# Performance work log

Measured on AMD Instinct MI355X. Metric: run time of the kernel, lower is better.

Reference implementation:

```python
import jax, jax.numpy as jnp
import numpy as np

D, A, B, R, N, E, NENT, L = 128, 64, 8, 200, 100000, 800000, 50000, 2
SLOPE = (0.125 + 1.0 / 3.0) / 2.0  # RReLU eval-mode slope (lower+upper)/2
EPS = 1e-5


def _ln(x, g, b):
    mu = jnp.mean(x, axis=-1, keepdims=True)
    v = jnp.mean((x - mu) ** 2, axis=-1, keepdims=True)
    return (x - mu) * jax.lax.rsqrt(v + EPS) * g + b


def _rrelu(x):
    return jnp.where(x >= 0, x, SLOPE * x)


def setup_inputs() -> dict:
    key = jax.random.key(0)
    ks = jax.random.split(key, 32)
    s = 0.05
    inp = {
        'hidden': jax.random.normal(ks[0], (N, D), jnp.float32),
        'rel_emb': jax.random.normal(ks[1], (B * (R + 1), D), jnp.float32),
        'batch_idx': jax.random.randint(ks[2], (E,), 0, B, jnp.int32),
        'rel': jax.random.randint(ks[3], (E,), 0, R + 1, jnp.int32),
        'sub': jax.random.randint(ks[4], (E,), 0, N, jnp.int32),
        'obj': jax.random.randint(ks[5], (E,), 0, N, jnp.int32),
        'q_rel': jax.random.randint(ks[6], (B,), 0, R + 1, jnp.int32),
        'nodes_batch': jax.random.randint(ks[7], (N,), 0, B, jnp.int32),
        'nodes_ent': jax.random.randint(ks[8], (N,), 0, NENT, jnp.int32),
        # per-layer params (stacked over L); stored as [in, out]
        'Ws': jax.random.normal(ks[9], (L, D, A)) * s,
        'Wr': jax.random.normal(ks[10], (L, D, A)) * s,
        'Wqr_w': jax.random.normal(ks[11], (L, D, A)) * s,
        'Wqr_b': jnp.zeros((L, A)),
        'Walpha_w': jax.random.normal(ks[12], (L, A)) * s,
        'Walpha_b': jnp.zeros((L,)),
        'Wh': jax.random.normal(ks[13], (L, D, D)) * s,
        'rt_w': jax.random.normal(ks[14], (L, D, D)) * s,
        'rt_b': jnp.zeros((L, D)),
        'ln_g': jnp.ones((L, D)), 'ln_b': jnp.zeros((L, D)),
        'lnr_g': jnp.ones((L, D)), 'lnr_b': jnp.zeros((L, D)),
        # shared GRU (PyTorch layout: [3D, D], gates r,z,n)
        'gru_wih': jax.random.normal(ks[15], (3 * D, D)) * s,
        'gru_whh': jax.random.normal(ks[16], (3 * D, D)) * s,
        'gru_bih': jnp.zeros((3 * D,)),
        'gru_bhh': jnp.zeros((3 * D,)),
        'Wfinal': jax.random.normal(ks[17], (D,)) * s,
    }
    return inp


def _gru_step(x, h, wih, whh, bih, bhh):
    gi = x @ wih.T + bih
    gh = h @ whh.T + bhh
    i_r, i_z, i_n = jnp.split(gi, 3, axis=-1)
    h_r, h_z, h_n = jnp.split(gh, 3, axis=-1)
    r = jax.nn.sigmoid(i_r + h_r)
    z = jax.nn.sigmoid(i_z + h_z)
    n = jnp.tanh(i_n + r * h_n)
    return (1.0 - z) * n + z * h


def reference(hidden, rel_emb, Ws, Wr, Wqr_w, Wqr_b, Walpha_w, Walpha_b, Wh,
              rt_w, rt_b, ln_g, ln_b, lnr_g, lnr_b,
              gru_wih, gru_whh, gru_bih, gru_bhh, Wfinal,
              batch_idx, rel, sub, obj, q_rel, nodes_batch, nodes_ent):
    h0 = jnp.zeros_like(hidden)
    rel_flat_idx = rel + batch_idx * (R + 1)  # [E]
    q_flat_idx = q_rel + jnp.arange(B, dtype=q_rel.dtype) * (R + 1)  # [B]
    for i in range(L):
        # relation transfer + residual + LN
        re_ = jax.nn.relu(rel_emb @ rt_w[i] + rt_b[i])
        rel_emb = _ln(rel_emb + re_, lnr_g[i], lnr_b[i])
        # GNN layer: edge-wise gather
        hs = hidden[sub]                       # [E, D]
        hr = rel_emb[rel_flat_idx]             # [E, D]
        h_qr = rel_emb[q_flat_idx][batch_idx]  # [E, D]
        pre = hs @ Ws[i] + hr @ Wr[i] + h_qr @ Wqr_w[i] + Wqr_b[i]  # [E, A]
        alpha = jax.nn.sigmoid(_rrelu(pre) @ Walpha_w[i] + Walpha_b[i])  # [E]
        msg = alpha[:, None] * (hs + hr)       # [E, D]
        agg = jax.ops.segment_sum(msg, obj, num_segments=N)  # [N, D]
        hidden = _rrelu(agg @ Wh[i])
        hidden = _ln(hidden, ln_g[i], ln_b[i])
        hidden = _gru_step(hidden, h0, gru_wih, gru_whh, gru_bih, gru_bhh)
        h0 = hidden
        rel_emb = _ln(rel_emb, lnr_g[i], lnr_b[i])
    scores = hidden @ Wfinal  # [N]
    scores_all = jnp.zeros((B, NENT), dtype=scores.dtype).at[nodes_batch, nodes_ent].set(scores)
    return scores_all
```

## Files before the change

kernel.cpp:

```cpp
#include <hip/hip_runtime.h>
#include <hip/hip_bf16.h>

constexpr int DD = 128;
constexpr int AA = 64;
constexpr int GG = 384;
constexpr int XPAD = 136;
constexpr int GTS = 192;

#define SLOPE_F 0.22916666666666666f
#define LNEPS   1e-5f

typedef __attribute__((ext_vector_type(8))) short short8;
typedef __attribute__((ext_vector_type(4))) float f32x4;

static __device__ __forceinline__ float wave_sum(float v){
#pragma unroll
  for (int off = 32; off > 0; off >>= 1) v += __shfl_xor(v, off, 64);
  return v;
}
static __device__ __forceinline__ float red16(float v){
#pragma unroll
  for (int off = 1; off < 16; off <<= 1) v += __shfl_xor(v, off, 64);
  return v;
}
static __device__ __forceinline__ float sigm(float x){ return 1.0f / (1.0f + __expf(-x)); }
static __device__ __forceinline__ float fast_tanh(float x){
  float ax = fabsf(x);
  float t = __expf(-2.0f * ax);
  float r = (1.0f - t) / (1.0f + t);
  return copysignf(r, x);
}
static __device__ __forceinline__ float rrelu_f(float x){ return x >= 0.0f ? x : SLOPE_F * x; }
static __device__ __forceinline__ short bf16b(float f){
  __hip_bfloat16 h = __float2bfloat16(f);
  return *reinterpret_cast<short*>(&h);
}
static __device__ __forceinline__ float b2f_lo(unsigned int x){
  return __uint_as_float(x << 16);
}
static __device__ __forceinline__ float b2f_hi(unsigned int x){
  return __uint_as_float(x & 0xffff0000u);
}
static __device__ __forceinline__ short8 ld_frag_f32(const float* p){
  float4 f0 = *(const float4*)p;
  float4 f1 = *(const float4*)(p + 4);
  short8 v;
  v[0]=bf16b(f0.x); v[1]=bf16b(f0.y); v[2]=bf16b(f0.z); v[3]=bf16b(f0.w);
  v[4]=bf16b(f1.x); v[5]=bf16b(f1.y); v[6]=bf16b(f1.z); v[7]=bf16b(f1.w);
  return v;
}

template<bool PRE_LN>
__global__ void __launch_bounds__(256) k_rel_transfer(float* __restrict__ rel,
    const float* __restrict__ rtw, const float* __restrict__ rtb,
    const float* __restrict__ g, const float* __restrict__ b,
    const float* __restrict__ gp, const float* __restrict__ bp, int rows){
  __shared__ float xrow[4][DD];
  float* xl = xrow[threadIdx.x >> 6];
  const int lane = threadIdx.x & 63;
  int wave = (int)((blockIdx.x * blockDim.x + threadIdx.x) >> 6);
  if (wave >= rows) return;
  int row = __builtin_amdgcn_readfirstlane(wave);
  float* x = rel + (size_t)row * DD;
  float t0 = x[lane], t1 = x[64 + lane];
  if (PRE_LN){
    float mu = wave_sum(t0 + t1) * (1.0f/128.0f);
    float e0 = t0 - mu, e1 = t1 - mu;
    float var = wave_sum(e0*e0 + e1*e1) * (1.0f/128.0f);
    float rs = rsqrtf(var + LNEPS);
    t0 = e0 * rs * gp[lane]      + bp[lane];
    t1 = e1 * rs * gp[64 + lane] + bp[64 + lane];
  }
  xl[lane] = t0; xl[64 + lane] = t1;
  float y0 = 0.f, y1 = 0.f;
#pragma unroll 4
  for (int d = 0; d < DD; ++d){
    float xd = xl[d];
    y0 = fmaf(xd, rtw[d*DD + lane],      y0);
    y1 = fmaf(xd, rtw[d*DD + 64 + lane], y1);
  }
  float u0 = t0 + fmaxf(y0 + rtb[lane],      0.f);
  float u1 = t1 + fmaxf(y1 + rtb[64 + lane], 0.f);
  float mu = wave_sum(u0 + u1) * (1.0f/128.0f);
  float e0 = u0 - mu, e1 = u1 - mu;
  float var = wave_sum(e0*e0 + e1*e1) * (1.0f/128.0f);
  float rs = rsqrtf(var + LNEPS);
  x[lane]      = e0 * rs * g[lane]      + b[lane];
  x[64 + lane] = e1 * rs * g[64 + lane] + b[64 + lane];
}

__global__ void __launch_bounds__(256) k_prep_bfrag_km(const float* __restrict__ W,
    short* __restrict__ out, int C, int ldc){
  int idx = blockIdx.x * blockDim.x + threadIdx.x;
  int total = (C >> 4) * 4 * 64;
  if (idx >= total) return;
  int lane = idx & 63, ks = (idx >> 6) & 3, ct = idx >> 8;
  int k = ks*32 + ((lane >> 4) << 3);
  int c = (ct << 4) + (lane & 15);
  short8 v;
#pragma unroll
  for (int j = 0; j < 8; ++j) v[j] = bf16b(W[(size_t)(k + j)*ldc + c]);
  *reinterpret_cast<short8*>(out + (size_t)idx * 8) = v;
}

__global__ void __launch_bounds__(256) k_prep_bfrag(const float* __restrict__ W,
    short* __restrict__ out, int Nc){
  int idx = blockIdx.x * blockDim.x + threadIdx.x;
  int total = (Nc >> 4) * 4 * 64;
  if (idx >= total) return;
  int lane = idx & 63, ks = (idx >> 6) & 3, ct = idx >> 8;
  int k = ks*32 + ((lane >> 4) << 3);
  int c = (ct << 4) + (lane & 15);
  const float* src = W + (size_t)c * DD + k;
  short8 v;
#pragma unroll
  for (int j = 0; j < 8; ++j) v[j] = bf16b(src[j]);
  *reinterpret_cast<short8*>(out + (size_t)idx * 8) = v;
}

__global__ void __launch_bounds__(256) k_proj_gt(const float* __restrict__ X,
    const short* __restrict__ Bf, unsigned short* __restrict__ GT, int rows){
  const int lane = threadIdx.x & 63;
  int wave = (int)((blockIdx.x * blockDim.x + threadIdx.x) >> 6);
  int r0 = wave * 16;
  if (r0 >= rows) return;
  if (r0 + 16 > rows) r0 = rows - 16;
  r0 = __builtin_amdgcn_readfirstlane(r0);
  const int arow = lane & 15;
  const int koff = (lane >> 4) << 3;
  short8 ax[4];
#pragma unroll
  for (int ks = 0; ks < 4; ++ks){
    ax[ks] = ld_frag_f32(X + (size_t)(r0 + arow) * DD + ks*32 + koff);
    *reinterpret_cast<short8*>((short*)GT + (size_t)(r0 + arow) * GTS + 64 + ks*32 + koff) = ax[ks];
  }
  f32x4 acc[4];
#pragma unroll
  for (int ct = 0; ct < 4; ++ct){
    acc[ct] = (f32x4)0.f;
#pragma unroll
    for (int ks = 0; ks < 4; ++ks){
      short8 bw = *reinterpret_cast<const short8*>(Bf + ((size_t)(ct*4 + ks)*64 + lane)*8);
      acc[ct] = __builtin_amdgcn_mfma_f32_16x16x32_bf16(ax[ks], bw, acc[ct], 0, 0, 0);
    }
  }
#pragma unroll
  for (int ct = 0; ct < 4; ++ct){
    int col = ct*16 + (lane & 15);
#pragma unroll
    for (int reg = 0; reg < 4; ++reg){
      int row = r0 + ((lane >> 4) << 2) + reg;
      ((short*)GT)[(size_t)row*GTS + col] = bf16b(acc[ct][reg]);
    }
  }
}

__global__ void __launch_bounds__(256) k_projq(const float* __restrict__ rel,
    const float* __restrict__ Wqr, const float* __restrict__ bias,
    const int* __restrict__ q_rel, float* __restrict__ out, int Bc, int Rp1){
  const int lane = threadIdx.x & 63;
  int wave = (int)((blockIdx.x * blockDim.x + threadIdx.x) >> 6);
  if (wave >= Bc) return;
  int b = __builtin_amdgcn_readfirstlane(wave);
  int f = __builtin_amdgcn_readfirstlane(q_rel[b] + b * Rp1);
  const float* x = rel + (size_t)f * DD;
  float a = 0.f;
#pragma unroll 4
  for (int d = 0; d < DD; ++d) a = fmaf(x[d], Wqr[d*AA + lane], a);
  out[(size_t)b*AA + lane] = a + bias[lane];
}

__global__ void __launch_bounds__(256) k_hist(const int* __restrict__ obj, int* __restrict__ deg, int E){
  int idx = blockIdx.x * blockDim.x + threadIdx.x;
  if (idx < E) atomicAdd(&deg[obj[idx]], 1);
}

__global__ void __launch_bounds__(1024) k_scan1(const int* __restrict__ deg,
    int* __restrict__ row_start, int* __restrict__ bsum, int n){
  __shared__ int sm[1024];
  int t = threadIdx.x;
  int i = blockIdx.x * 1024 + t;
  int v = (i < n) ? deg[i] : 0;
  sm[t] = v; __syncthreads();
#pragma unroll
  for (int off = 1; off < 1024; off <<= 1){
    int x = (t >= off) ? sm[t - off] : 0;
    __syncthreads();
    sm[t] += x;
    __syncthreads();
  }
  if (i < n) row_start[i] = sm[t] - v;
  if (t == 1023) bsum[blockIdx.x] = sm[1023];
}

__global__ void __launch_bounds__(1024) k_scan2(int* __restrict__ bsum, int nb){
  __shared__ int sm[1024];
  int t = threadIdx.x;
  int v = (t < nb) ? bsum[t] : 0;
  sm[t] = v; __syncthreads();
#pragma unroll
  for (int off = 1; off < 1024; off <<= 1){
    int x = (t >= off) ? sm[t - off] : 0;
    __syncthreads();
    sm[t] += x;
    __syncthreads();
  }
  if (t < nb) bsum[t] = sm[t] - v;
}

__global__ void __launch_bounds__(256) k_scan3(int* __restrict__ row_start,
    const int* __restrict__ bsum, int n, int E){
  int i = blockIdx.x * blockDim.x + threadIdx.x;
  if (i < n) row_start[i] += bsum[i >> 10];
  if (i == 0) row_start[n] = E;
}

__global__ void __launch_bounds__(256) k_scatter_edges(const int* __restrict__ obj,
    const int* __restrict__ sub, const int* __restrict__ bidx,
    const int* __restrict__ reli, const int* __restrict__ row_start,
    int* __restrict__ cursor, unsigned int* __restrict__ ER, int E, int Rp1){
  int e = blockIdx.x * blockDim.x + threadIdx.x;
  if (e < E){
    int o = obj[e];
    int pos = row_start[o] + atomicAdd(&cursor[o], 1);
    int bb = bidx[e];
    unsigned rec = (unsigned)sub[e] | ((unsigned)(reli[e] + bb * Rp1) << 17)
                 | ((unsigned)bb << 28);
    ER[pos] = rec;
  }
}

__global__ void __launch_bounds__(256) k_edge_csr4(
    const unsigned short* __restrict__ GT, const unsigned short* __restrict__ RT,
    const float* __restrict__ qr,
    const float* __restrict__ wal, const float* __restrict__ walb_p,
    const unsigned int* __restrict__ ER, const int* __restrict__ row_start,
    float* __restrict__ agg, int Nn){
  const int lane = threadIdx.x & 63;
  const int g = lane >> 4;
  const int t = lane & 15;
  int wave = (int)((blockIdx.x * blockDim.x + threadIdx.x) >> 6);
  if (wave >= Nn) return;
  int o = __builtin_amdgcn_readfirstlane(wave);
  const int s0 = __builtin_amdgcn_readfirstlane(row_start[o]);
  const int s1 = __builtin_amdgcn_readfirstlane(row_start[o + 1]);
  const float4 wa4 = *reinterpret_cast<const float4*>(wal + t*4);
  const float wb = walb_p[0];
  float acc[8];
#pragma unroll
  for (int i = 0; i < 8; ++i) acc[i] = 0.f;
  for (int base = s0; base < s1; base += 8){
    int pA = base + g;
    int pB = base + g + 4;
    bool vA = pA < s1, vB = pB < s1;
    unsigned eA = ER[vA ? pA : s0];
    unsigned eB = ER[vB ? pB : s0];
    int sA = eA & 0x1FFFF, fA = (eA >> 17) & 0x7FF, bA = eA >> 28;
    int sB = eB & 0x1FFFF, fB = (eB >> 17) & 0x7FF, bB = eB >> 28;
    const unsigned short* gsA = GT + (size_t)sA * GTS;
    const unsigned short* rfA = RT + (size_t)fA * GTS;
    const unsigned short* gsB = GT + (size_t)sB * GTS;
    const unsigned short* rfB = RT + (size_t)fB * GTS;
    uint2 pgA = *reinterpret_cast<const uint2*>(gsA + t*4);
    uint2 prA = *reinterpret_cast<const uint2*>(rfA + t*4);
    float4 q4A = *reinterpret_cast<const float4*>(qr + (size_t)bA*AA + t*4);
    uint4 xgA = *reinterpret_cast<const uint4*>(gsA + 64 + t*8);
    uint4 xrA = *reinterpret_cast<const uint4*>(rfA + 64 + t*8);
    uint2 pgB = *reinterpret_cast<const uint2*>(gsB + t*4);
    uint2 prB = *reinterpret_cast<const uint2*>(rfB + t*4);
    float4 q4B = *reinterpret_cast<const float4*>(qr + (size_t)bB*AA + t*4);
    uint4 xgB = *reinterpret_cast<const uint4*>(gsB + 64 + t*8);
    uint4 xrB = *reinterpret_cast<const uint4*>(rfB + 64 + t*8);
    float pA0 = b2f_lo(pgA.x) + b2f_lo(prA.x) + q4A.x;
    float pA1 = b2f_hi(pgA.x) + b2f_hi(prA.x) + q4A.y;
    float pA2 = b2f_lo(pgA.y) + b2f_lo(prA.y) + q4A.z;
    float pA3 = b2f_hi(pgA.y) + b2f_hi(prA.y) + q4A.w;
    float dotA = rrelu_f(pA0)*wa4.x + rrelu_f(pA1)*wa4.y
               + rrelu_f(pA2)*wa4.z + rrelu_f(pA3)*wa4.w;
    float pB0 = b2f_lo(pgB.x) + b2f_lo(prB.x) + q4B.x;
    float pB1 = b2f_hi(pgB.x) + b2f_hi(prB.x) + q4B.y;
    float pB2 = b2f_lo(pgB.y) + b2f_lo(prB.y) + q4B.z;
    float pB3 = b2f_hi(pgB.y) + b2f_hi(prB.y) + q4B.w;
    float dotB = rrelu_f(pB0)*wa4.x + rrelu_f(pB1)*wa4.y
               + rrelu_f(pB2)*wa4.z + rrelu_f(pB3)*wa4.w;
#pragma unroll
    for (int off = 1; off < 16; off <<= 1){
      dotA += __shfl_xor(dotA, off, 64);
      dotB += __shfl_xor(dotB, off, 64);
    }
    float alA = vA ? sigm(dotA + wb) : 0.f;
    float alB = vB ? sigm(dotB + wb) : 0.f;
    acc[0] = fmaf(alA, b2f_lo(xgA.x) + b2f_lo(xrA.x), fmaf(alB, b2f_lo(xgB.x) + b2f_lo(xrB.x), acc[0]));
    acc[1] = fmaf(alA, b2f_hi(xgA.x) + b2f_hi(xrA.x), fmaf(alB, b2f_hi(xgB.x) + b2f_hi(xrB.x), acc[1]));
    acc[2] = fmaf(alA, b2f_lo(xgA.y) + b2f_lo(xrA.y), fmaf(alB, b2f_lo(xgB.y) + b2f_lo(xrB.y), acc[2]));
    acc[3] = fmaf(alA, b2f_hi(xgA.y) + b2f_hi(xrA.y), fmaf(alB, b2f_hi(xgB.y) + b2f_hi(xrB.y), acc[3]));
    acc[4] = fmaf(alA, b2f_lo(xgA.z) + b2f_lo(xrA.z), fmaf(alB, b2f_lo(xgB.z) + b2f_lo(xrB.z), acc[4]));
    acc[5] = fmaf(alA, b2f_hi(xgA.z) + b2f_hi(xrA.z), fmaf(alB, b2f_hi(xgB.z) + b2f_hi(xrB.z), acc[5]));
    acc[6] = fmaf(alA, b2f_lo(xgA.w) + b2f_lo(xrA.w), fmaf(alB, b2f_lo(xgB.w) + b2f_lo(xrB.w), acc[6]));
    acc[7] = fmaf(alA, b2f_hi(xgA.w) + b2f_hi(xrA.w), fmaf(alB, b2f_hi(xgB.w) + b2f_hi(xrB.w), acc[7]));
  }
#pragma unroll
  for (int i = 0; i < 8; ++i){
    acc[i] += __shfl_xor(acc[i], 16, 64);
    acc[i] += __shfl_xor(acc[i], 32, 64);
  }
  if (g == 0){
    float4 v0 = make_float4(acc[0], acc[1], acc[2], acc[3]);
    float4 v1 = make_float4(acc[4], acc[5], acc[6], acc[7]);
    *reinterpret_cast<float4*>(agg + (size_t)o*DD + t*8)     = v0;
    *reinterpret_cast<float4*>(agg + (size_t)o*DD + t*8 + 4) = v1;
  }
}

template<bool HAS_H>
__global__ void __launch_bounds__(256) k_whlngru(const float* __restrict__ AGG,
    float* H, const short* __restrict__ Bwh, const short* __restrict__ Bih,
    const short* __restrict__ Bhh, const float* __restrict__ lng,
    const float* __restrict__ lnb, const float* __restrict__ bih,
    const float* __restrict__ bhh, int rows){
  __shared__ short xtile[4 * 16 * XPAD];
  __shared__ short wbuf[2][12 * 512];
  short* xl = xtile + (threadIdx.x >> 6) * 16 * XPAD;
  const int lane = threadIdx.x & 63;
  const int wib  = threadIdx.x >> 6;
  int wave = (int)((blockIdx.x * blockDim.x + threadIdx.x) >> 6);
  const bool live = (wave * 16 < rows);
  int r0 = live ? wave * 16 : 0;
  if (r0 + 16 > rows) r0 = rows - 16;
  r0 = __builtin_amdgcn_readfirstlane(r0);
  const int arow = lane & 15;
  const int koff = (lane >> 4) << 3;
  const int lrbase = (lane >> 4) << 2;
  constexpr int NU = HAS_H ? 16 : 8;

  auto stage = [&](int u, int par){
    int ct = HAS_H ? (u >> 1) : u;
    const short* src = (HAS_H && (u & 1)) ? Bhh : Bih;
#pragma unroll
    for (int jj = 0; jj < 3; ++jj){
      int j = wib * 3 + jj;
      int gfrag = (j >> 2) * 32 + ct * 4 + (j & 3);
      *reinterpret_cast<short8*>(&wbuf[par][j * 512 + lane * 8]) =
          *reinterpret_cast<const short8*>(src + (size_t)gfrag * 512 + lane * 8);
    }
  };

  stage(0, 0);

  short8 aa[4];
#pragma unroll
  for (int ks = 0; ks < 4; ++ks)
    aa[ks] = ld_frag_f32(AGG + (size_t)(r0 + arow) * DD + ks*32 + koff);
  f32x4 acc[8];
#pragma unroll
  for (int ct = 0; ct < 8; ++ct){
    acc[ct] = (f32x4)0.f;
#pragma unroll
    for (int ks = 0; ks < 4; ++ks){
      short8 bw = *reinterpret_cast<const short8*>(Bwh + ((size_t)(ct*4 + ks)*64 + lane)*8);
      acc[ct] = __builtin_amdgcn_mfma_f32_16x16x32_bf16(aa[ks], bw, acc[ct], 0, 0, 0);
    }
  }
#pragma unroll
  for (int ct = 0; ct < 8; ++ct)
#pragma unroll
    for (int reg = 0; reg < 4; ++reg) acc[ct][reg] = rrelu_f(acc[ct][reg]);

  float mu[4], rs[4];
#pragma unroll
  for (int reg = 0; reg < 4; ++reg){
    float s = 0.f, ss = 0.f;
#pragma unroll
    for (int ct = 0; ct < 8; ++ct){ float v = acc[ct][reg]; s += v; ss += v*v; }
    s = red16(s); ss = red16(ss);
    float m = s * (1.0f/128.0f);
    float var = ss * (1.0f/128.0f) - m*m;
    mu[reg] = m;
    rs[reg] = rsqrtf(var + LNEPS);
  }
#pragma unroll
  for (int ct = 0; ct < 8; ++ct){
    int col = ct*16 + (lane & 15);
    float gv = lng[col], bv = lnb[col];
#pragma unroll
    for (int reg = 0; reg < 4; ++reg){
      float xn = (acc[ct][reg] - mu[reg]) * rs[reg] * gv + bv;
      xl[(lrbase + reg) * XPAD + col] = bf16b(xn);
    }
  }

  short8 ax[4], ah8[4];
#pragma unroll
  for (int ks = 0; ks < 4; ++ks)
    ax[ks] = *reinterpret_cast<const short8*>(&xl[arow * XPAD + ks*32 + koff]);
  if (HAS_H){
#pragma unroll
    for (int ks = 0; ks < 4; ++ks)
      ah8[ks] = ld_frag_f32(H + (size_t)(r0 + arow) * DD + ks*32 + koff);
  }

  __syncthreads();

  f32x4 air = (f32x4)0.f, aiz = (f32x4)0.f, ain = (f32x4)0.f;
  f32x4 ahr = (f32x4)0.f, ahz = (f32x4)0.f, ahn = (f32x4)0.f;
#pragma unroll
  for (int u = 0; u < NU; ++u){
    if (u + 1 < NU) stage(u + 1, (u + 1) & 1);
    const short* wb = wbuf[u & 1];
    const bool is_hh = HAS_H && (u & 1);
    const int ct = HAS_H ? (u >> 1) : u;
    if (!is_hh){
      air = (f32x4)0.f; aiz = (f32x4)0.f; ain = (f32x4)0.f;
      ahr = (f32x4)0.f; ahz = (f32x4)0.f; ahn = (f32x4)0.f;
    }
#pragma unroll
    for (int ks = 0; ks < 4; ++ks){
      short8 b0 = *reinterpret_cast<const short8*>(&wb[(0*4 + ks)*512 + lane*8]);
      short8 b1 = *reinterpret_cast<const short8*>(&wb[(1*4 + ks)*512 + lane*8]);
      short8 b2 = *reinterpret_cast<const short8*>(&wb[(2*4 + ks)*512 + lane*8]);
      if (!is_hh){
        air = __builtin_amdgcn_mfma_f32_16x16x32_bf16(ax[ks], b0, air, 0, 0, 0);
        aiz = __builtin_amdgcn_mfma_f32_16x16x32_bf16(ax[ks], b1, aiz, 0, 0, 0);
        ain = __builtin_amdgcn_mfma_f32_16x16x32_bf16(ax[ks], b2, ain, 0, 0, 0);
      } else {
        ahr = __builtin_amdgcn_mfma_f32_16x16x32_bf16(ah8[ks], b0, ahr, 0, 0, 0);
        ahz = __builtin_amdgcn_mfma_f32_16x16x32_bf16(ah8[ks], b1, ahz, 0, 0, 0);
        ahn = __builtin_amdgcn_mfma_f32_16x16x32_bf16(ah8[ks], b2, ahn, 0, 0, 0);
      }
    }
    if (!HAS_H || is_hh){
      int col = ct*16 + (lane & 15);
      float bi_r = bih[col], bi_z = bih[128 + col], bi_n = bih[256 + col];
      float bh_r = bhh[col], bh_z = bhh[128 + col], bh_n = bhh[256 + col];
#pragma unroll
      for (int reg = 0; reg < 4; ++reg){
        int row = r0 + lrbase + reg;
        float gi_r = air[reg] + bi_r;
        float gi_z = aiz[reg] + bi_z;
        float gi_n = ain[reg] + bi_n;
        float gh_r = (HAS_H ? ahr[reg] : 0.f) + bh_r;
        float gh_z = (HAS_H ? ahz[reg] : 0.f) + bh_z;
        float gh_n = (HAS_H ? ahn[reg] : 0.f) + bh_n;
        float rg = sigm(gi_r + gh_r);
        float zg = sigm(gi_z + gh_z);
        float ng = fast_tanh(gi_n + rg * gh_n);
        float hp = HAS_H ? H[(size_t)row * DD + col] : 0.f;
        if (live) H[(size_t)row * DD + col] = (1.f - zg) * ng + zg * hp;
      }
    }
    __syncthreads();
  }
}

__global__ void __launch_bounds__(256) k_score(const float* __restrict__ Hf,
    const float* __restrict__ wf, const int* __restrict__ nb, const int* __restrict__ ne,
    float* __restrict__ scores, int* __restrict__ winner, int rows, int NENT){
  const int lane = threadIdx.x & 63;
  int wave = (int)((blockIdx.x * blockDim.x + threadIdx.x) >> 6);
  if (wave >= rows) return;
  int row = __builtin_amdgcn_readfirstlane(wave);
  float v = Hf[(size_t)row*DD + lane] * wf[lane] + Hf[(size_t)row*DD + 64 + lane] * wf[64 + lane];
  float s = wave_sum(v);
  if (lane == 0){
    scores[row] = s;
    int slot = nb[row] * NENT + ne[row];
    atomicMax(&winner[slot], row);
  }
}

__global__ void __launch_bounds__(256) k_scatter(const float* __restrict__ scores,
    const int* __restrict__ winner, const int* __restrict__ nb, const int* __restrict__ ne,
    float* __restrict__ out, int rows, int NENT){
  int n = blockIdx.x * blockDim.x + threadIdx.x;
  if (n < rows){
    int slot = nb[n] * NENT + ne[n];
    if (winner[slot] == n) out[slot] = scores[n];
  }
}

extern "C" void kernel_launch(void* const* d_in, const int* in_sizes, int n_in,
                              void* d_out, int out_size, void* d_ws, size_t ws_size,
                              hipStream_t stream){
  const float* hidden0 = (const float*)d_in[0];
  const float* rel0    = (const float*)d_in[1];
  const int* batch_idx = (const int*)d_in[2];
  const int* rel_i     = (const int*)d_in[3];
  const int* sub       = (const int*)d_in[4];
  const int* obj       = (const int*)d_in[5];
  const int* q_rel     = (const int*)d_in[6];
  const int* nb        = (const int*)d_in[7];
  const int* ne        = (const int*)d_in[8];
  const float* Ws      = (const float*)d_in[9];
  const float* Wr      = (const float*)d_in[10];
  const float* Wqr_w   = (const float*)d_in[11];
  const float* Wqr_b   = (const float*)d_in[12];
  const float* Wal_w   = (const float*)d_in[13];
  const float* Wal_b   = (const float*)d_in[14];
  const float* Wh      = (const float*)d_in[15];
  const float* rt_w    = (const float*)d_in[16];
  const float* rt_b    = (const float*)d_in[17];
  const float* ln_g    = (const float*)d_in[18];
  const float* ln_b    = (const float*)d_in[19];
  const float* lnr_g   = (const float*)d_in[20];
  const float* lnr_b   = (const float*)d_in[21];
  const float* wih     = (const float*)d_in[22];
  const float* whh     = (const float*)d_in[23];
  const float* bih     = (const float*)d_in[24];
  const float* bhh     = (const float*)d_in[25];
  const float* wfin    = (const float*)d_in[26];

  const int N    = in_sizes[0] / DD;
  const int NR   = in_sizes[1] / DD;
  const int E    = in_sizes[2];
  const int Bc   = in_sizes[6];
  const int L    = in_sizes[14];
  const int Rp1  = NR / Bc;
  const int NENT = out_size / Bc;

  char* wsp = (char*)d_ws;
  auto alloc = [&](size_t bytes) -> void* {
    void* p = (void*)wsp;
    wsp += (bytes + 255) & ~(size_t)255;
    return p;
  };
  float* AGG     = (float*)alloc((size_t)N * DD * 4);
  float* HBUF    = (float*)alloc((size_t)N * DD * 4);
  float* rel_cur = (float*)alloc((size_t)NR * DD * 4);
  unsigned short* GT = (unsigned short*)alloc((size_t)N * GTS * 2);
  unsigned short* RT = (unsigned short*)alloc((size_t)NR * GTS * 2);
  float* qr      = (float*)alloc((size_t)Bc * AA * 4);
  short* Bih     = (short*)alloc((size_t)(GG/16) * 4 * 64 * 8 * 2);
  short* Bhh     = (short*)alloc((size_t)(GG/16) * 4 * 64 * 8 * 2);
  short* Bws     = (short*)alloc((size_t)L * 4 * 4 * 64 * 8 * 2);
  short* Bwr     = (short*)alloc((size_t)L * 4 * 4 * 64 * 8 * 2);
  short* Bwh     = (short*)alloc((size_t)L * 8 * 4 * 64 * 8 * 2);
  float* scores  = (float*)alloc((size_t)N * 4);
  int*   winner  = (int*)alloc((size_t)Bc * NENT * 4);
  int*   deg     = (int*)alloc((size_t)N * 4);
  int*   row_st  = (int*)alloc((size_t)(N + 1) * 4);
  int*   cursor  = (int*)alloc((size_t)N * 4);
  unsigned int* ER = (unsigned int*)alloc((size_t)E * 4);
  int*   bsum    = (int*)alloc((size_t)1024 * 4);
  (void)ws_size; (void)n_in;

  hipMemcpyAsync(rel_cur, rel0, (size_t)NR * DD * 4, hipMemcpyDeviceToDevice, stream);
  {
    int totg = (GG/16) * 4 * 64;
    k_prep_bfrag<<<(totg + 255)/256, 256, 0, stream>>>(wih, Bih, GG);
    k_prep_bfrag<<<(totg + 255)/256, 256, 0, stream>>>(whh, Bhh, GG);
    int tot64 = 4 * 4 * 64;
    int tot128 = 8 * 4 * 64;
    for (int i = 0; i < L; ++i){
      k_prep_bfrag_km<<<(tot64 + 255)/256, 256, 0, stream>>>(Ws + (size_t)i*DD*AA, Bws + (size_t)i*tot64*8, AA, AA);
      k_prep_bfrag_km<<<(tot64 + 255)/256, 256, 0, stream>>>(Wr + (size_t)i*DD*AA, Bwr + (size_t)i*tot64*8, AA, AA);
      k_prep_bfrag_km<<<(tot128 + 255)/256, 256, 0, stream>>>(Wh + (size_t)i*DD*DD, Bwh + (size_t)i*tot128*8, DD, DD);
    }
  }
  hipMemsetAsync(d_out, 0, (size_t)out_size * 4, stream);
  hipMemsetAsync(winner, 0xFF, (size_t)Bc * NENT * 4, stream);

  hipMemsetAsync(deg, 0, (size_t)N * 4, stream);
  hipMemsetAsync(cursor, 0, (size_t)N * 4, stream);
  k_hist<<<(E + 255)/256, 256, 0, stream>>>(obj, deg, E);
  {
    int nb1 = (N + 1023)/1024;
    k_scan1<<<nb1, 1024, 0, stream>>>(deg, row_st, bsum, N);
    k_scan2<<<1, 1024, 0, stream>>>(bsum, nb1);
    k_scan3<<<(N + 255)/256, 256, 0, stream>>>(row_st, bsum, N, E);
  }
  k_scatter_edges<<<(E + 255)/256, 256, 0, stream>>>(obj, sub, batch_idx, rel_i,
      row_st, cursor, ER, E, Rp1);

  const float* hid_in = hidden0;
  auto blocks4 = [](int waves){ return (waves + 3) / 4; };
  const int tot64 = 4 * 4 * 64;
  const int tot128 = 8 * 4 * 64;

  for (int i = 0; i < L; ++i){
    if (i == 0)
      k_rel_transfer<false><<<blocks4(NR), 256, 0, stream>>>(rel_cur,
          rt_w + (size_t)i*DD*DD, rt_b + (size_t)i*DD,
          lnr_g + (size_t)i*DD, lnr_b + (size_t)i*DD,
          nullptr, nullptr, NR);
    else
      k_rel_transfer<true><<<blocks4(NR), 256, 0, stream>>>(rel_cur,
          rt_w + (size_t)i*DD*DD, rt_b + (size_t)i*DD,
          lnr_g + (size_t)i*DD, lnr_b + (size_t)i*DD,
          lnr_g + (size_t)(i-1)*DD, lnr_b + (size_t)(i-1)*DD, NR);
    k_proj_gt<<<blocks4((N+15)/16), 256, 0, stream>>>(hid_in, Bws + (size_t)i*tot64*8, GT, N);
    k_proj_gt<<<blocks4((NR+15)/16), 256, 0, stream>>>(rel_cur, Bwr + (size_t)i*tot64*8, RT, NR);
    k_projq<<<blocks4(Bc), 256, 0, stream>>>(rel_cur, Wqr_w + (size_t)i*DD*AA,
        Wqr_b + (size_t)i*AA, q_rel, qr, Bc, Rp1);
    k_edge_csr4<<<blocks4(N), 256, 0, stream>>>(GT, RT, qr,
        Wal_w + (size_t)i*AA, Wal_b + i, ER, row_st, AGG, N);
    {
      int waves = (N + 15)/16;
      if (i == 0)
        k_whlngru<false><<<blocks4(waves), 256, 0, stream>>>(AGG, HBUF,
            Bwh + (size_t)i*tot128*8, Bih, Bhh,
            ln_g + (size_t)i*DD, ln_b + (size_t)i*DD, bih, bhh, N);
      else
        k_whlngru<true><<<blocks4(waves), 256, 0, stream>>>(AGG, HBUF,
            Bwh + (size_t)i*tot128*8, Bih, Bhh,
            ln_g + (size_t)i*DD, ln_b + (size_t)i*DD, bih, bhh, N);
    }
    hid_in = HBUF;
  }

  k_score<<<blocks4(N), 256, 0, stream>>>(hid_in, wfin, nb, ne, scores, winner, N, NENT);
  k_scatter<<<(N + 255)/256, 256, 0, stream>>>(scores, winner, nb, ne, (float*)d_out, N, NENT);
}
```

Measured before the change: 473.4 us.

## Fuse next-layer projection and final scoring into Wh/LN/GRU kernel

The GRU kernel now keeps its output hidden tile in LDS as bf16 and either computes the next layer's Ws projection and bf16 hidden copy into GT directly, or computes final scores and the winner atomics. This removes the separate k_proj_gt launch for later layers and the k_score kernel, along with the re-read of H from global memory. In the last layer H is no longer written at all. The GRU loop also stages the input and hidden gate weights together, halving the loop trips at the cost of doubled LDS weight buffers, which may lower occupancy. Scores are now computed from bf16-rounded hidden values, a small precision change.

```diff
diff --git a/kernel.cpp b/kernel.cpp
--- a/kernel.cpp
+++ b/kernel.cpp
@@ -40,6 +40,9 @@
 }
 static __device__ __forceinline__ float b2f_hi(unsigned int x){
   return __uint_as_float(x & 0xffff0000u);
+}
+static __device__ __forceinline__ float b2f_s(short s){
+  return __uint_as_float(((unsigned int)(unsigned short)s) << 16);
 }
 static __device__ __forceinline__ short8 ld_frag_f32(const float* p){
   float4 f0 = *(const float4*)p;
@@ -312,14 +315,20 @@
   }
 }
 
-template<bool HAS_H>
+template<bool HAS_H, bool PROJ, bool SCORE>
 __global__ void __launch_bounds__(256) k_whlngru(const float* __restrict__ AGG,
     float* H, const short* __restrict__ Bwh, const short* __restrict__ Bih,
     const short* __restrict__ Bhh, const float* __restrict__ lng,
     const float* __restrict__ lnb, const float* __restrict__ bih,
-    const float* __restrict__ bhh, int rows){
+    const float* __restrict__ bhh,
+    const short* __restrict__ Bproj, unsigned short* __restrict__ GT,
+    const float* __restrict__ wf, const int* __restrict__ nbp,
+    const int* __restrict__ nep, float* __restrict__ scores,
+    int* __restrict__ winner, int NENT, int rows){
+  constexpr int UF = HAS_H ? 24 : 12;
+  constexpr int FPW = HAS_H ? 6 : 3;
   __shared__ short xtile[4 * 16 * XPAD];
-  __shared__ short wbuf[2][12 * 512];
+  __shared__ short wbuf[2][UF * 512];
   short* xl = xtile + (threadIdx.x >> 6) * 16 * XPAD;
   const int lane = threadIdx.x & 63;
   const int wib  = threadIdx.x >> 6;
@@ -331,15 +340,15 @@
   const int arow = lane & 15;
   const int koff = (lane >> 4) << 3;
   const int lrbase = (lane >> 4) << 2;
-  constexpr int NU = HAS_H ? 16 : 8;
 
   auto stage = [&](int u, int par){
-    int ct = HAS_H ? (u >> 1) : u;
-    const short* src = (HAS_H && (u & 1)) ? Bhh : Bih;
-#pragma unroll
-    for (int jj = 0; jj < 3; ++jj){
-      int j = wib * 3 + jj;
-      int gfrag = (j >> 2) * 32 + ct * 4 + (j & 3);
+    int ct = u;
+#pragma unroll
+    for (int jj = 0; jj < FPW; ++jj){
+      int j = wib * FPW + jj;
+      int jl = (j < 12) ? j : j - 12;
+      const short* src = (HAS_H && j >= 12) ? Bhh : Bih;
+      int gfrag = (jl >> 2) * 32 + ct * 4 + (jl & 3);
       *reinterpret_cast<short8*>(&wbuf[par][j * 512 + lane * 8]) =
           *reinterpret_cast<const short8*>(src + (size_t)gfrag * 512 + lane * 8);
     }
@@ -401,35 +410,31 @@
 
   __syncthreads();
 
-  f32x4 air = (f32x4)0.f, aiz = (f32x4)0.f, ain = (f32x4)0.f;
-  f32x4 ahr = (f32x4)0.f, ahz = (f32x4)0.f, ahn = (f32x4)0.f;
-#pragma unroll
-  for (int u = 0; u < NU; ++u){
-    if (u + 1 < NU) stage(u + 1, (u + 1) & 1);
+#pragma unroll
+  for (int u = 0; u < 8; ++u){
+    if (u + 1 < 8) stage(u + 1, (u + 1) & 1);
     const short* wb = wbuf[u & 1];
-    const bool is_hh = HAS_H && (u & 1);
-    const int ct = HAS_H ? (u >> 1) : u;
-    if (!is_hh){
-      air = (f32x4)0.f; aiz = (f32x4)0.f; ain = (f32x4)0.f;
-      ahr = (f32x4)0.f; ahz = (f32x4)0.f; ahn = (f32x4)0.f;
-    }
+    f32x4 air = (f32x4)0.f, aiz = (f32x4)0.f, ain = (f32x4)0.f;
+    f32x4 ahr = (f32x4)0.f, ahz = (f32x4)0.f, ahn = (f32x4)0.f;
 #pragma unroll
     for (int ks = 0; ks < 4; ++ks){
       short8 b0 = *reinterpret_cast<const short8*>(&wb[(0*4 + ks)*512 + lane*8]);
       short8 b1 = *reinterpret_cast<const short8*>(&wb[(1*4 + ks)*512 + lane*8]);
       short8 b2 = *reinterpret_cast<const short8*>(&wb[(2*4 + ks)*512 + lane*8]);
-      if (!is_hh){
-        air = __builtin_amdgcn_mfma_f32_16x16x32_bf16(ax[ks], b0, air, 0, 0, 0);
-        aiz = __builtin_amdgcn_mfma_f32_16x16x32_bf16(ax[ks], b1, aiz, 0, 0, 0);
-        ain = __builtin_amdgcn_mfma_f32_16x16x32_bf16(ax[ks], b2, ain, 0, 0, 0);
-      } else {
-        ahr = __builtin_amdgcn_mfma_f32_16x16x32_bf16(ah8[ks], b0, ahr, 0, 0, 0);
-        ahz = __builtin_amdgcn_mfma_f32_16x16x32_bf16(ah8[ks], b1, ahz, 0, 0, 0);
-        ahn = __builtin_amdgcn_mfma_f32_16x16x32_bf16(ah8[ks], b2, ahn, 0, 0, 0);
+      air = __builtin_amdgcn_mfma_f32_16x16x32_bf16(ax[ks], b0, air, 0, 0, 0);
+      aiz = __builtin_amdgcn_mfma_f32_16x16x32_bf16(ax[ks], b1, aiz, 0, 0, 0);
+      ain = __builtin_amdgcn_mfma_f32_16x16x32_bf16(ax[ks], b2, ain, 0, 0, 0);
+      if (HAS_H){
+        short8 c0 = *reinterpret_cast<const short8*>(&wb[(12 + 0*4 + ks)*512 + lane*8]);
+        short8 c1 = *reinterpret_cast<const short8*>(&wb[(12 + 1*4 + ks)*512 + lane*8]);
+        short8 c2 = *reinterpret_cast<const short8*>(&wb[(12 + 2*4 + ks)*512 + lane*8]);
+        ahr = __builtin_amdgcn_mfma_f32_16x16x32_bf16(ah8[ks], c0, ahr, 0, 0, 0);
+        ahz = __builtin_amdgcn_mfma_f32_16x16x32_bf16(ah8[ks], c1, ahz, 0, 0, 0);
+        ahn = __builtin_amdgcn_mfma_f32_16x16x32_bf16(ah8[ks], c2, ahn, 0, 0, 0);
       }
     }
-    if (!HAS_H || is_hh){
-      int col = ct*16 + (lane & 15);
+    {
+      int col = u*16 + (lane & 15);
       float bi_r = bih[col], bi_z = bih[128 + col], bi_n = bih[256 + col];
       float bh_r = bhh[col], bh_z = bhh[128 + col], bh_n = bhh[256 + col];
 #pragma unroll
@@ -445,26 +450,64 @@
         float zg = sigm(gi_z + gh_z);
         float ng = fast_tanh(gi_n + rg * gh_n);
         float hp = HAS_H ? H[(size_t)row * DD + col] : 0.f;
-        if (live) H[(size_t)row * DD + col] = (1.f - zg) * ng + zg * hp;
+        float hv = (1.f - zg) * ng + zg * hp;
+        if (!SCORE && live) H[(size_t)row * DD + col] = hv;
+        if (PROJ || SCORE) xl[(lrbase + reg) * XPAD + col] = bf16b(hv);
       }
     }
     __syncthreads();
   }
-}
-
-__global__ void __launch_bounds__(256) k_score(const float* __restrict__ Hf,
-    const float* __restrict__ wf, const int* __restrict__ nb, const int* __restrict__ ne,
-    float* __restrict__ scores, int* __restrict__ winner, int rows, int NENT){
-  const int lane = threadIdx.x & 63;
-  int wave = (int)((blockIdx.x * blockDim.x + threadIdx.x) >> 6);
-  if (wave >= rows) return;
-  int row = __builtin_amdgcn_readfirstlane(wave);
-  float v = Hf[(size_t)row*DD + lane] * wf[lane] + Hf[(size_t)row*DD + 64 + lane] * wf[64 + lane];
-  float s = wave_sum(v);
-  if (lane == 0){
-    scores[row] = s;
-    int slot = nb[row] * NENT + ne[row];
-    atomicMax(&winner[slot], row);
+
+  if (PROJ || SCORE){
+    short8 hx[4];
+#pragma unroll
+    for (int ks = 0; ks < 4; ++ks)
+      hx[ks] = *reinterpret_cast<const short8*>(&xl[arow * XPAD + ks*32 + koff]);
+    if (PROJ){
+      if (live){
+#pragma unroll
+        for (int ks = 0; ks < 4; ++ks)
+          *reinterpret_cast<short8*>((short*)GT + (size_t)(r0 + arow) * GTS + 64 + ks*32 + koff) = hx[ks];
+      }
+      f32x4 pacc[4];
+#pragma unroll
+      for (int ct = 0; ct < 4; ++ct){
+        pacc[ct] = (f32x4)0.f;
+#pragma unroll
+        for (int ks = 0; ks < 4; ++ks){
+          short8 bw = *reinterpret_cast<const short8*>(Bproj + ((size_t)(ct*4 + ks)*64 + lane)*8);
+          pacc[ct] = __builtin_amdgcn_mfma_f32_16x16x32_bf16(hx[ks], bw, pacc[ct], 0, 0, 0);
+        }
+      }
+      if (live){
+#pragma unroll
+        for (int ct = 0; ct < 4; ++ct){
+          int col = ct*16 + (lane & 15);
+#pragma unroll
+          for (int reg = 0; reg < 4; ++reg){
+            int row = r0 + lrbase + reg;
+            ((short*)GT)[(size_t)row*GTS + col] = bf16b(pacc[ct][reg]);
+          }
+        }
+      }
+    }
+    if (SCORE){
+      float part = 0.f;
+#pragma unroll
+      for (int ks = 0; ks < 4; ++ks){
+#pragma unroll
+        for (int j = 0; j < 8; ++j)
+          part = fmaf(b2f_s(hx[ks][j]), wf[ks*32 + koff + j], part);
+      }
+      part += __shfl_xor(part, 16, 64);
+      part += __shfl_xor(part, 32, 64);
+      if (live && (lane >> 4) == 0){
+        int row = r0 + arow;
+        scores[row] = part;
+        int slot = nbp[row] * NENT + nep[row];
+        atomicMax(&winner[slot], row);
+      }
+    }
   }
 }
 
@@ -571,7 +614,6 @@
   k_scatter_edges<<<(E + 255)/256, 256, 0, stream>>>(obj, sub, batch_idx, rel_i,
       row_st, cursor, ER, E, Rp1);
 
-  const float* hid_in = hidden0;
   auto blocks4 = [](int waves){ return (waves + 3) / 4; };
   const int tot64 = 4 * 4 * 64;
   const int tot128 = 8 * 4 * 64;
@@ -587,7 +629,8 @@
           rt_w + (size_t)i*DD*DD, rt_b + (size_t)i*DD,
           lnr_g + (size_t)i*DD, lnr_b + (size_t)i*DD,
           lnr_g + (size_t)(i-1)*DD, lnr_b + (size_t)(i-1)*DD, NR);
-    k_proj_gt<<<blocks4((N+15)/16), 256, 0, stream>>>(hid_in, Bws + (size_t)i*tot64*8, GT, N);
+    if (i == 0)
+      k_proj_gt<<<blocks4((N+15)/16), 256, 0, stream>>>(hidden0, Bws, GT, N);
     k_proj_gt<<<blocks4((NR+15)/16), 256, 0, stream>>>(rel_cur, Bwr + (size_t)i*tot64*8, RT, NR);
     k_projq<<<blocks4(Bc), 256, 0, stream>>>(rel_cur, Wqr_w + (size_t)i*DD*AA,
         Wqr_b + (size_t)i*AA, q_rel, qr, Bc, Rp1);
@@ -595,18 +638,28 @@
         Wal_w + (size_t)i*AA, Wal_b + i, ER, row_st, AGG, N);
     {
       int waves = (N + 15)/16;
-      if (i == 0)
-        k_whlngru<false><<<blocks4(waves), 256, 0, stream>>>(AGG, HBUF,
-            Bwh + (size_t)i*tot128*8, Bih, Bhh,
-            ln_g + (size_t)i*DD, ln_b + (size_t)i*DD, bih, bhh, N);
+      int blocks = blocks4(waves);
+      const bool has_h = (i > 0);
+      const bool proj  = (i + 1 < L);
+      const bool score = (i == L - 1);
+      const short* Bp = proj ? (Bws + (size_t)(i+1)*tot64*8) : nullptr;
+      const float* lg = ln_g + (size_t)i*DD;
+      const float* lb = ln_b + (size_t)i*DD;
+      const short* Bw = Bwh + (size_t)i*tot128*8;
+      if (!has_h && proj && !score)
+        k_whlngru<false,true,false><<<blocks, 256, 0, stream>>>(AGG, HBUF, Bw, Bih, Bhh,
+            lg, lb, bih, bhh, Bp, GT, wfin, nb, ne, scores, winner, NENT, N);
+      else if (!has_h && !proj && score)
+        k_whlngru<false,false,true><<<blocks, 256, 0, stream>>>(AGG, HBUF, Bw, Bih, Bhh,
+            lg, lb, bih, bhh, Bp, GT, wfin, nb, ne, scores, winner, NENT, N);
+      else if (has_h && proj && !score)
+        k_whlngru<true,true,false><<<blocks, 256, 0, stream>>>(AGG, HBUF, Bw, Bih, Bhh,
+            lg, lb, bih, bhh, Bp, GT, wfin, nb, ne, scores, winner, NENT, N);
       else
-        k_whlngru<true><<<blocks4(waves), 256, 0, stream>>>(AGG, HBUF,
-            Bwh + (size_t)i*tot128*8, Bih, Bhh,
-            ln_g + (size_t)i*DD, ln_b + (size_t)i*DD, bih, bhh, N);
-    }
-    hid_in = HBUF;
-  }
-
-  k_score<<<blocks4(N), 256, 0, stream>>>(hid_in, wfin, nb, ne, scores, winner, N, NENT);
+        k_whlngru<true,false,true><<<blocks, 256, 0, stream>>>(AGG, HBUF, Bw, Bih, Bhh,
+            lg, lb, bih, bhh, Bp, GT, wfin, nb, ne, scores, winner, NENT, N);
+    }
+  }
+
   k_scatter<<<(N + 255)/256, 256, 0, stream>>>(scores, winner, nb, ne, (float*)d_out, N, NENT);
 }
```

Result: faster. 459.6 us (-2.9%).
